# Kernel tuning notes

Measured on AMD Instinct MI355X. Metric: run time of the kernel, lower is better.

The kernel has to match this reference:

```python
import jax, jax.numpy as jnp
import numpy as np
import math

N_HEADS = 16
ROPE_BASE = 10000.0


def rotate_half(x):
    x1 = x[..., ::2]
    x2 = x[..., 1::2]
    return jnp.stack((-x2, x1), axis=-1).reshape(x.shape)


def rope_tables(seq_len, head_dim, dtype):
    inv_freq = 1.0 / (ROPE_BASE ** (jnp.arange(0, head_dim, 2, dtype=jnp.float32) / head_dim))
    positions = jnp.arange(seq_len, dtype=jnp.float32)
    freqs = jnp.outer(positions, inv_freq)            # [S, hd/2]
    emb = jnp.concatenate((freqs, freqs), axis=-1)    # [S, hd]  (matches torch cat convention)
    cos = jnp.cos(emb)[None, None, :, :].astype(dtype)
    sin = jnp.sin(emb)[None, None, :, :].astype(dtype)
    return cos, sin


def setup_inputs() -> dict:
    key = jax.random.key(0)
    k1, k2, k3 = jax.random.split(key, 3)
    B, S, D = 2, 2048, 1024
    x = jax.random.normal(k1, (B, S, D), dtype=jnp.float32)
    # causal lower-triangular mask, broadcastable over batch and heads
    mask = jnp.tril(jnp.ones((S, S), dtype=jnp.int32))[None, None, :, :]
    w_qkv = jax.random.normal(k2, (D, 3 * D), dtype=jnp.float32) * 0.02
    w_out = jax.random.normal(k3, (D, D), dtype=jnp.float32) * 0.02
    return {"x": x, "mask": mask, "w_qkv": w_qkv, "w_out": w_out}


def reference(x, mask, w_qkv, w_out):
    B, S, D = x.shape
    H = N_HEADS
    hd = D // H
    qkv = (x @ w_qkv).reshape(B, S, 3, H, hd)
    qkv = jnp.transpose(qkv, (2, 0, 3, 1, 4))         # [3, B, H, S, hd]
    q, k, v = qkv[0], qkv[1], qkv[2]
    cos, sin = rope_tables(S, hd, x.dtype)
    q = q * cos + rotate_half(q) * sin
    k = k * cos + rotate_half(k) * sin
    scale = math.sqrt(hd)
    attn = jnp.einsum("bhsd,bhtd->bhst", q, k) / scale
    attn = jnp.where(mask == 0, -jnp.inf, attn)
    attn = jax.nn.softmax(attn, axis=-1)              # dropout p=0.0 -> identity
    out = jnp.einsum("bhst,bhtd->bhsd", attn, v)
    out = jnp.transpose(out, (0, 2, 1, 3)).reshape(B, S, D)
    return out @ w_out
```

## Files before the change

kernel.cpp:

```cpp
#include <hip/hip_runtime.h>
#include <stdint.h>

typedef unsigned short u16;
typedef __bf16 bf16x8 __attribute__((ext_vector_type(8)));
typedef float f32x4 __attribute__((ext_vector_type(4)));

#define S_LEN 2048
#define NH    16
#define DM    1024
#define N3    3072
#define MROWS 4096

__device__ __forceinline__ float b2f(u16 u) {
  unsigned int v = ((unsigned int)u) << 16;
  return __builtin_bit_cast(float, v);
}
__device__ __forceinline__ u16 f2b(float f) {
  unsigned int v = __builtin_bit_cast(unsigned int, f);
  v += 0x7fffu + ((v >> 16) & 1u);
  return (u16)(v >> 16);
}
__device__ __forceinline__ u16 f2b_trunc(float f) {
  return (u16)(__builtin_bit_cast(unsigned int, f) >> 16);
}
__device__ __forceinline__ bf16x8 ld8(const u16* p) { return *(const bf16x8*)p; }
__device__ __forceinline__ f32x4 mfma16(bf16x8 a, bf16x8 b, f32x4 c) {
  return __builtin_amdgcn_mfma_f32_16x16x32_bf16(a, b, c, 0, 0, 0);
}
__device__ __forceinline__ void glds16(const void* g, void* l) {
  __builtin_amdgcn_global_load_lds(
      (const __attribute__((address_space(1))) unsigned int*)g,
      (__attribute__((address_space(3))) unsigned int*)l, 16, 0, 0);
}
__device__ __forceinline__ int bfish(unsigned int w) {
  unsigned int e = (w >> 7) & 0xffu;
  return (e >= 100u && e <= 134u) ? 1 : 0;
}

__global__ __launch_bounds__(256) void prep_kernel(const void* __restrict__ x,
                                                   const void* __restrict__ wqkv,
                                                   const void* __restrict__ wout,
                                                   u16* __restrict__ xb,
                                                   u16* __restrict__ wqT,
                                                   u16* __restrict__ woT,
                                                   float* __restrict__ cs,
                                                   int* __restrict__ flag) {
  const int bx = blockIdx.x;
  const int t = threadIdx.x;
  if (bx < 2048) {
    __shared__ int cnt;
    if (t == 0) cnt = 0;
    __syncthreads();
    size_t i = (size_t)bx * 256 + t;
    const uint4* xv = (const uint4*)x;
    uint4 probe = xv[i];
    unsigned int wds[4]; *(uint4*)wds = probe;
    atomicAdd(&cnt, bfish(wds[0]) + bfish(wds[1]) + bfish(wds[2]) + bfish(wds[3]));
    __syncthreads();
    const int isbf = cnt > 512;
    if (t == 0) *flag = isbf;
    if (isbf) {
      ((uint4*)xb)[i] = probe;
    } else {
      const float4* xf4 = (const float4*)x;
      uint2* xb2 = (uint2*)xb;
      #pragma unroll
      for (int half = 0; half < 2; ++half) {
        const size_t idx = (size_t)bx * 512 + half * 256 + t;
        const float4 v = xf4[idx];
        u16 pk[4];
        pk[0] = f2b(v.x); pk[1] = f2b(v.y); pk[2] = f2b(v.z); pk[3] = f2b(v.w);
        xb2[idx] = *(const uint2*)pk;
      }
    }
    return;
  }
  if (bx < 2560) {
    int i = (bx - 2048) * 256 + t;
    int s = i >> 6, d = i & 63;
    int f = d & 31;
    float invf = expf(-(float)(2 * f) * (1.0f / 64.0f) * logf(10000.0f));
    float th = (float)s * invf;
    float sv, cv;
    sincosf(th, &sv, &cv);
    cs[i * 2] = cv; cs[i * 2 + 1] = sv;
    return;
  }
  const int wq = bx < 3328;
  const int id = wq ? (bx - 2560) : (bx - 3328);
  const int ncx = wq ? 48 : 16;
  const void* in = wq ? wqkv : wout;
  u16* out = wq ? wqT : woT;
  const int C = wq ? 3072 : 1024;
  const int c0 = (id % ncx) * 64, r0 = (id / ncx) * 64;
  __shared__ int cnt;
  __shared__ u16 L[4096];
  if (t == 0) cnt = 0;
  __syncthreads();
  const unsigned int* wv = (const unsigned int*)in;
  size_t off = (((size_t)id) * 256 + t) & 262143;
  atomicAdd(&cnt, bfish(wv[off]));
  __syncthreads();
  const int fl = cnt > 128;
  if (fl) {
    #pragma unroll
    for (int it = 0; it < 2; ++it) {
      int c = it * 256 + t;
      int rl = c >> 3, cseg = c & 7;
      uint4 v = *(const uint4*)((const u16*)in + (size_t)(r0 + rl) * C + c0 + cseg * 8);
      u16 e[8]; *(uint4*)e = v;
      #pragma unroll
      for (int jj = 0; jj < 8; ++jj) {
        int cl = cseg * 8 + jj;
        L[cl * 64 + (rl ^ (cseg << 3))] = e[jj];
      }
    }
  } else {
    const float* inf_ = (const float*)in;
    #pragma unroll
    for (int it = 0; it < 16; ++it) {
      int c = it * 256 + t;
      int rl = c >> 6, cl = c & 63;
      L[cl * 64 + (rl ^ ((cl >> 3) << 3))] = f2b(inf_[(size_t)(r0 + rl) * C + c0 + cl]);
    }
  }
  __syncthreads();
  #pragma unroll
  for (int it = 0; it < 2; ++it) {
    int c = it * 256 + t;
    int cl = c >> 3, rseg = c & 7;
    uint4 v = *(const uint4*)(L + cl * 64 + (((rseg ^ (cl >> 3)) & 7) << 3));
    *(uint4*)(out + (size_t)(c0 + cl) * 1024 + r0 + rseg * 8) = v;
  }
}


#define PHASE_PRE() do { \
  asm volatile("" ::: "memory"); \
  __builtin_amdgcn_s_barrier(); \
  asm volatile("s_waitcnt lgkmcnt(0)" ::: "memory"); \
  __builtin_amdgcn_sched_barrier(0); \
  __builtin_amdgcn_s_setprio(1); \
} while (0)

#define PHASE_POST() do { \
  __builtin_amdgcn_s_setprio(0); \
  asm volatile("" ::: "memory"); \
  __builtin_amdgcn_s_barrier(); \
} while (0)

#define LOADA(P) \
  _Pragma("unroll") \
  for (int ii = 0; ii < 2; ++ii) { \
    const int row = wr * 128 + ((P) * 2 + ii) * 16 + ln; \
    _Pragma("unroll") \
    for (int kk = 0; kk < 2; ++kk) \
      a[ii][kk] = ld8(Ap + row * 64 + (((kk * 4 + quad) ^ (row & 7)) << 3)); \
  }

#define MFMAQ(P) \
  _Pragma("unroll") \
  for (int ii = 0; ii < 2; ++ii) { \
    _Pragma("unroll") \
    for (int j = 0; j < 4; ++j) { \
      acc[(P) * 2 + ii][j] = mfma16(a[ii][0], b[j][0], acc[(P) * 2 + ii][j]); \
      acc[(P) * 2 + ii][j] = mfma16(a[ii][1], b[j][1], acc[(P) * 2 + ii][j]); \
    } \
  }

__global__ __launch_bounds__(512, 2) void gemm_qkv(const u16* __restrict__ A,
                                                   const u16* __restrict__ Bt,
                                                   u16* __restrict__ Qo,
                                                   u16* __restrict__ Ko,
                                                   u16* __restrict__ Vt,
                                                   const float* __restrict__ cs) {
  __shared__ u16 smem[2][32768];
  const int t = threadIdx.x;
  const int lane = t & 63, wave = t >> 6;
  const int ln = lane & 15, quad = lane >> 4;
  const int wr = wave >> 2, wc = wave & 3;
  const int m0 = blockIdx.x * 256, n0 = blockIdx.y * 256;
  const u16* gA0 = A + (size_t)m0 * 1024;
  const u16* gA1 = A + (size_t)(m0 + 128) * 1024;
  const u16* gB0 = Bt + (size_t)n0 * 1024;
  const u16* gB1 = Bt + (size_t)(n0 + 128) * 1024;
  f32x4 acc[8][4] = {};

  auto stage_half = [&](u16* lds, const u16* g, int k0) {
    #pragma unroll
    for (int it = 0; it < 2; ++it) {
      const int c = it * 512 + t;
      const int row = c >> 3, sg = (c & 7) ^ (row & 7);
      glds16(g + (size_t)row * 1024 + k0 + sg * 8, (char*)lds + c * 16);
    }
  };

  stage_half(&smem[0][0],     gA0, 0);
  stage_half(&smem[0][8192],  gA1, 0);
  stage_half(&smem[0][16384], gB0, 0);
  stage_half(&smem[0][24576], gB1, 0);
  stage_half(&smem[1][16384], gB0, 64);
  stage_half(&smem[1][24576], gB1, 64);
  asm volatile("s_waitcnt vmcnt(4)" ::: "memory");
  __builtin_amdgcn_s_barrier();

  for (int kt = 0; kt < 16; ++kt) {
    const int p = kt & 1;
    u16* Ap = &smem[p][0];
    u16* Bp = &smem[p][16384];
    u16* Aq = &smem[p ^ 1][0];
    const int kA = (kt + 1) * 64, kB = (kt + 2) * 64;
    bf16x8 b[4][2], a[2][2];
    #pragma unroll
    for (int j = 0; j < 4; ++j) {
      const int row = wc * 64 + j * 16 + ln;
      #pragma unroll
      for (int kk = 0; kk < 2; ++kk)
        b[j][kk] = ld8(Bp + row * 64 + (((kk * 4 + quad) ^ (row & 7)) << 3));
    }
    LOADA(0);
    if (kt < 15) stage_half(Aq, gA0, kA);
    PHASE_PRE(); MFMAQ(0); PHASE_POST();
    LOADA(1);
    if (kt < 15) stage_half(Aq + 8192, gA1, kA);
    PHASE_PRE(); MFMAQ(1); PHASE_POST();
    LOADA(2);
    if (kt < 14) stage_half(Bp, gB0, kB);
    PHASE_PRE(); MFMAQ(2); PHASE_POST();
    LOADA(3);
    if (kt < 14) stage_half(Bp + 8192, gB1, kB);
    PHASE_PRE(); MFMAQ(3);
    __builtin_amdgcn_s_setprio(0);
    if (kt < 14) { asm volatile("s_waitcnt vmcnt(4)" ::: "memory"); }
    else         { asm volatile("s_waitcnt vmcnt(0)" ::: "memory"); }
    asm volatile("" ::: "memory");
    __builtin_amdgcn_s_barrier();
  }

  u16* Tl = &smem[0][0];
  const int which = n0 >> 10;
  const int b_ = m0 >> 11;
  const int s0 = m0 & 2047;
  const int h0 = (n0 & 1023) >> 6;

  if (which < 2) {
    const float qs = which ? 1.0f : 0.18033688011112042f;
    const float2* cs2 = (const float2*)cs;
    #pragma unroll
    for (int i = 0; i < 8; ++i) {
      const int slb = wr * 128 + i * 16 + quad * 4;
      #pragma unroll
      for (int j = 0; j < 4; ++j) {
        const int c = wc * 64 + j * 16 + ln;
        const int d = c & 63;
        const float sgn = (d & 1) ? 1.0f : -1.0f;
        #pragma unroll
        for (int r = 0; r < 4; ++r) {
          const int sl = slb + r;
          const float v = acc[i][j][r];
          const float pp = __shfl_xor(v, 1);
          const float2 cv = cs2[(size_t)(s0 + sl) * 64 + d];
          const float val = (v * cv.x + sgn * pp * cv.y) * qs;
          *(u16*)((char*)Tl + sl * 512 + ((((c >> 3) + 4 * (sl & 7)) & 31) << 4)
                  + ((c & 7) << 1)) = f2b(val);
        }
      }
    }
    __syncthreads();
    u16* dst = which ? Ko : Qo;
    #pragma unroll
    for (int it = 0; it < 16; ++it) {
      const int g = it * 512 + t;
      const int c3 = g & 7, sl = (g >> 3) & 255, h = g >> 11;
      const int ch = h * 8 + c3;
      const uint4 vv = *(const uint4*)((const char*)Tl + sl * 512
                        + (((ch + 4 * (sl & 7)) & 31) << 4));
      *(uint4*)(dst + ((size_t)(b_ * NH + h0 + h) * S_LEN + s0 + sl) * 64 + c3 * 8) = vv;
    }
  } else {
    #pragma unroll
    for (int i = 0; i < 8; ++i) {
      const int slb = wr * 128 + i * 16 + quad * 4;
      #pragma unroll
      for (int j = 0; j < 4; ++j) {
        const int c = wc * 64 + j * 16 + ln;
        u16 pk[4];
        #pragma unroll
        for (int r = 0; r < 4; ++r) pk[r] = f2b(acc[i][j][r]);
        *(uint2*)((char*)Tl + c * 512 + ((((slb >> 3) + c) & 31) << 4)
                  + ((slb & 7) << 1)) = *(const uint2*)pk;
      }
    }
    __syncthreads();
    #pragma unroll
    for (int it = 0; it < 16; ++it) {
      const int g = it * 512 + t;
      const int sc = g & 31, cd = g >> 5;
      const int h = cd >> 6, d = cd & 63;
      const uint4 vv = *(const uint4*)((const char*)Tl + cd * 512
                        + (((sc + cd) & 31) << 4));
      *(uint4*)(&Vt[((size_t)((b_ * NH + h0 + h) * 64 + d)) * S_LEN + s0 + sc * 8]) = vv;
    }
  }
}

#undef PHASE_PRE
#undef PHASE_POST
#undef LOADA
#undef MFMAQ

__global__ __launch_bounds__(256) void attn_kernel(const u16* __restrict__ Qb,
                                                   const u16* __restrict__ Kb,
                                                   const u16* __restrict__ Vt,
                                                   u16* __restrict__ Ao) {
  __shared__ u16 smem[20480];
  u16* Kl = smem;
  u16* Vl = smem + 8192;
  u16* Pl = smem + 16384;
  const int t = threadIdx.x;
  const int lane = t & 63, w = t >> 6;
  const int ln = lane & 15, quad = lane >> 4;
  const int i = blockIdx.x;
  const int xcd = i & 7;
  const int j = i >> 3;
  const int bh = (xcd << 2) | (j & 3);
  const int q5 = j >> 2;
  const int g = q5 & 7, s5 = q5 >> 3;
  const int qt = (s5 & 1) ? (31 - ((s5 >> 1) << 3) - g) : (((s5 >> 1) << 3) + g);
  const int q0 = qt * 64;
  const int b = bh >> 4, h = bh & 15;
  const u16* Qbh = Qb + (size_t)bh * (S_LEN * 64);
  const u16* Kbh = Kb + (size_t)bh * (S_LEN * 64);
  const u16* Vtbh = Vt + (size_t)bh * (64 * S_LEN);
  u16* Plw = Pl + w * 1024;
  u16* AoBase = Ao + (size_t)b * S_LEN * DM + h * 64;

  auto stage = [&](int kt, int bufi) {
    u16* kd = Kl + bufi * 4096;
    u16* vd = Vl + bufi * 4096;
    const u16* kg = Kbh + (size_t)kt * 64 * 64;
    const u16* vg = Vtbh + (size_t)kt * 64;
    #pragma unroll
    for (int it = 0; it < 2; ++it) {
      int c = it * 256 + t;
      int row = c >> 3, sg = (c & 7) ^ (row & 7);
      glds16((const char*)kg + ((size_t)row * 64 + sg * 8) * 2,   (char*)kd + c * 16);
      glds16((const char*)vg + ((size_t)row * 2048 + sg * 8) * 2, (char*)vd + c * 16);
    }
  };

  bf16x8 bq[2];
  #pragma unroll
  for (int kk = 0; kk < 2; ++kk)
    bq[kk] = ld8(Qbh + (size_t)(q0 + w * 16 + ln) * 64 + kk * 32 + quad * 8);

  f32x4 o[4] = {};
  float l = 0.f;

  stage(0, 0);
  __syncthreads();

  for (int kt = 0; kt <= qt; ++kt) {
    const int bufi = kt & 1;
    if (kt < qt) stage(kt + 1, bufi ^ 1);
    const u16* Kb_ = Kl + bufi * 4096;
    const u16* Vb_ = Vl + bufi * 4096;

    f32x4 st[4] = {};
    #pragma unroll
    for (int kk = 0; kk < 2; ++kk)
      #pragma unroll
      for (int ct = 0; ct < 4; ++ct) {
        bf16x8 ak = ld8(Kb_ + (ct * 16 + ln) * 64 + (((kk * 4 + quad) ^ (ln & 7)) << 3));
        st[ct] = mfma16(ak, bq[kk], st[ct]);
      }

    const bool diag = (kt == qt);
    #pragma unroll
    for (int ct = 0; ct < 4; ++ct) {
      u16 pk[4];
      #pragma unroll
      for (int r = 0; r < 4; ++r) {
        float p;
        if (diag && (ct * 16 + quad * 4 + r) > (w * 16 + ln)) p = 0.f;
        else p = __builtin_amdgcn_exp2f(st[ct][r]);
        l += p;
        pk[r] = f2b_trunc(p);
      }
      *(uint2*)(Plw + ln * 64 + ((((ct * 2) + (quad >> 1)) ^ (ln & 7)) << 3)
                + ((quad & 1) << 2)) = *(const uint2*)pk;
    }

    #pragma unroll
    for (int k4 = 0; k4 < 2; ++k4) {
      bf16x8 bp = ld8(Plw + ln * 64 + (((k4 * 4 + quad) ^ (ln & 7)) << 3));
      #pragma unroll
      for (int dt = 0; dt < 4; ++dt) {
        bf16x8 av = ld8(Vb_ + (dt * 16 + ln) * 64 + (((k4 * 4 + quad) ^ (ln & 7)) << 3));
        o[dt] = mfma16(av, bp, o[dt]);
      }
    }
    __syncthreads();
  }

  l += __shfl_xor(l, 16);
  l += __shfl_xor(l, 32);
  const float inv = 1.f / l;
  const size_t qrow = (size_t)(q0 + w * 16 + ln) * DM;
  #pragma unroll
  for (int dt = 0; dt < 4; ++dt) {
    u16 pk[4];
    #pragma unroll
    for (int r = 0; r < 4; ++r) pk[r] = f2b(o[dt][r] * inv);
    *(uint2*)(AoBase + qrow + dt * 16 + quad * 4) = *(const uint2*)pk;
  }
}

template <int TM>
__global__ __launch_bounds__(256) void gemm_out_t(const u16* __restrict__ A,
                                                  const u16* __restrict__ Bt,
                                                  void* __restrict__ Out,
                                                  const int* __restrict__ flag) {
  constexpr int MI = TM / 32;
  __shared__ u16 smem[(TM + 128) * 64];
  u16* Al = smem;
  u16* Bl = smem + TM * 64;
  const int t = threadIdx.x;
  const int lane = t & 63, wave = t >> 6;
  const int ln = lane & 15, quad = lane >> 4;
  const int wr = wave >> 1, wc = wave & 1;
  const int m0 = blockIdx.x * TM, n0 = blockIdx.y * 128;
  const char* Ab = (const char*)A;
  const char* Bb = (const char*)Bt;
  f32x4 acc[MI][4] = {};

  for (int k0 = 0; k0 < 1024; k0 += 64) {
    __syncthreads();
    #pragma unroll
    for (int it = 0; it < TM / 32; ++it) {
      const int c = it * 256 + t;
      const int row = c >> 3, sg = (c & 7) ^ (row & 7);
      glds16(Ab + ((size_t)(m0 + row) * 1024 + k0 + sg * 8) * 2, (char*)Al + c * 16);
    }
    #pragma unroll
    for (int it = 0; it < 4; ++it) {
      const int c = it * 256 + t;
      const int row = c >> 3, sg = (c & 7) ^ (row & 7);
      glds16(Bb + ((size_t)(n0 + row) * 1024 + k0 + sg * 8) * 2, (char*)Bl + c * 16);
    }
    __syncthreads();
    bf16x8 a[MI][2], b[4][2];
    #pragma unroll
    for (int i = 0; i < MI; ++i) {
      const int row = wr * (TM / 2) + i * 16 + ln;
      #pragma unroll
      for (int kk = 0; kk < 2; ++kk)
        a[i][kk] = ld8(Al + row * 64 + (((kk * 4 + quad) ^ (row & 7)) << 3));
    }
    #pragma unroll
    for (int j = 0; j < 4; ++j) {
      const int row = wc * 64 + j * 16 + ln;
      #pragma unroll
      for (int kk = 0; kk < 2; ++kk)
        b[j][kk] = ld8(Bl + row * 64 + (((kk * 4 + quad) ^ (row & 7)) << 3));
    }
    #pragma unroll
    for (int i = 0; i < MI; ++i)
      #pragma unroll
      for (int j = 0; j < 4; ++j) {
        acc[i][j] = mfma16(a[i][0], b[j][0], acc[i][j]);
        acc[i][j] = mfma16(a[i][1], b[j][1], acc[i][j]);
      }
  }

  const int fl = *flag;
  #pragma unroll
  for (int i = 0; i < MI; ++i)
    #pragma unroll
    for (int j = 0; j < 4; ++j)
      #pragma unroll
      for (int r = 0; r < 4; ++r) {
        int m = m0 + wr * (TM / 2) + i * 16 + quad * 4 + r;
        int c = n0 + wc * 64 + j * 16 + ln;
        float v = acc[i][j][r];
        if (fl) ((u16*)Out)[(size_t)m * DM + c] = f2b(v);
        else    ((float*)Out)[(size_t)m * DM + c] = v;
      }
}

extern "C" void kernel_launch(void* const* d_in, const int* in_sizes, int n_in,
                              void* d_out, int out_size, void* d_ws, size_t ws_size,
                              hipStream_t stream) {
  (void)in_sizes; (void)n_in; (void)out_size; (void)ws_size;
  const void* x    = d_in[0];
  const void* wqkv = d_in[2];
  const void* wout = d_in[3];
  char* ws = (char*)d_ws;
  u16*  xb   = (u16*)(ws + 0);
  u16*  Ao   = xb;
  u16*  wqT  = (u16*)(ws + 8388608);
  u16*  woT  = (u16*)(ws + 14680064);
  u16*  Qb   = (u16*)(ws + 16777216);
  u16*  Kb   = (u16*)(ws + 25165824);
  u16*  Vt   = (u16*)(ws + 33554432);
  float* cs  = (float*)(ws + 41943040);
  int*  flag = (int*)(ws + 42991616);

  prep_kernel<<<3584, 256, 0, stream>>>(x, wqkv, wout, xb, wqT, woT, cs, flag);
  gemm_qkv<<<dim3(16, 12), 512, 0, stream>>>(xb, wqT, Qb, Kb, Vt, cs);
  attn_kernel<<<1024, 256, 0, stream>>>(Qb, Kb, Vt, Ao);
  gemm_out_t<64><<<dim3(64, 8), 256, 0, stream>>>(Ao, woT, d_out, flag);
}
```

Baseline: 178.4 us.

## Load K and V directly from global memory in attention, drop LDS staging

Removes the double-buffered LDS staging of K and V tiles and the per-iteration block barrier. Each wave now reads K and V fragments straight from global memory, relying on the cache, since all four waves share the same tiles. Cutting LDS from 40KB to 8KB can raise occupancy. The cost is repeated global/L2 traffic per wave, no prefetch overlap, and V reads strided by sequence length.

After: 278.0 us. 55.8% more time.

```diff
diff --git a/kernel.cpp b/kernel.cpp
--- a/kernel.cpp
+++ b/kernel.cpp
@@ -313,10 +313,7 @@
                                                    const u16* __restrict__ Kb,
                                                    const u16* __restrict__ Vt,
                                                    u16* __restrict__ Ao) {
-  __shared__ u16 smem[20480];
-  u16* Kl = smem;
-  u16* Vl = smem + 8192;
-  u16* Pl = smem + 16384;
+  __shared__ u16 Pl[4096];
   const int t = threadIdx.x;
   const int lane = t & 63, w = t >> 6;
   const int ln = lane & 15, quad = lane >> 4;
@@ -335,20 +332,6 @@
   u16* Plw = Pl + w * 1024;
   u16* AoBase = Ao + (size_t)b * S_LEN * DM + h * 64;
 
-  auto stage = [&](int kt, int bufi) {
-    u16* kd = Kl + bufi * 4096;
-    u16* vd = Vl + bufi * 4096;
-    const u16* kg = Kbh + (size_t)kt * 64 * 64;
-    const u16* vg = Vtbh + (size_t)kt * 64;
-    #pragma unroll
-    for (int it = 0; it < 2; ++it) {
-      int c = it * 256 + t;
-      int row = c >> 3, sg = (c & 7) ^ (row & 7);
-      glds16((const char*)kg + ((size_t)row * 64 + sg * 8) * 2,   (char*)kd + c * 16);
-      glds16((const char*)vg + ((size_t)row * 2048 + sg * 8) * 2, (char*)vd + c * 16);
-    }
-  };
-
   bf16x8 bq[2];
   #pragma unroll
   for (int kk = 0; kk < 2; ++kk)
@@ -357,21 +340,16 @@
   f32x4 o[4] = {};
   float l = 0.f;
 
-  stage(0, 0);
-  __syncthreads();
-
   for (int kt = 0; kt <= qt; ++kt) {
-    const int bufi = kt & 1;
-    if (kt < qt) stage(kt + 1, bufi ^ 1);
-    const u16* Kb_ = Kl + bufi * 4096;
-    const u16* Vb_ = Vl + bufi * 4096;
+    const u16* Kt = Kbh + (size_t)kt * 64 * 64;
+    const u16* Vc = Vtbh + (size_t)kt * 64;
 
     f32x4 st[4] = {};
     #pragma unroll
     for (int kk = 0; kk < 2; ++kk)
       #pragma unroll
       for (int ct = 0; ct < 4; ++ct) {
-        bf16x8 ak = ld8(Kb_ + (ct * 16 + ln) * 64 + (((kk * 4 + quad) ^ (ln & 7)) << 3));
+        bf16x8 ak = ld8(Kt + (ct * 16 + ln) * 64 + (kk * 4 + quad) * 8);
         st[ct] = mfma16(ak, bq[kk], st[ct]);
       }
 
@@ -396,11 +374,10 @@
       bf16x8 bp = ld8(Plw + ln * 64 + (((k4 * 4 + quad) ^ (ln & 7)) << 3));
       #pragma unroll
       for (int dt = 0; dt < 4; ++dt) {
-        bf16x8 av = ld8(Vb_ + (dt * 16 + ln) * 64 + (((k4 * 4 + quad) ^ (ln & 7)) << 3));
+        bf16x8 av = ld8(Vc + (size_t)(dt * 16 + ln) * S_LEN + (k4 * 4 + quad) * 8);
         o[dt] = mfma16(av, bp, o[dt]);
       }
     }
-    __syncthreads();
   }
 
   l += __shfl_xor(l, 16);
```
